# Optimization experiments

Hardware: AMD Instinct MI355X
Metric: run time of the kernel (lower is better)

## Reference

```python
import jax, jax.numpy as jnp
import numpy as np

N_NODES = 100000
N_EDGES = 1200000
DIM = 64
MAX_DEG = 64
NUM_LAB = 16
BN_EPS = 1e-5


def _lrelu(x):
    return jax.nn.leaky_relu(x, negative_slope=0.01)


def _bn(x, g, b):
    # BatchNorm1d in training mode: batch statistics over node axis
    m = x.mean(axis=0)
    v = x.var(axis=0)
    return (x - m) * jax.lax.rsqrt(v + BN_EPS) * g + b


def _gin_layer(h, src, dst, n, w1, b1, w2, b2, eps, g, b):
    # GINConv: (1+eps)*x_i + sum_{j in N(i)} x_j, then MLP (lin_lrelu_lin), BN, LeakyReLU
    agg = jax.ops.segment_sum(h[src], dst, num_segments=n)
    x = (1.0 + eps) * h + agg
    x = _lrelu(x @ w1 + b1) @ w2 + b2
    return _lrelu(_bn(x, g, b))


def setup_inputs() -> dict:
    key = jax.random.key(0)
    ks = jax.random.split(key, 16)
    s = 0.05
    inp = {
        'node_deg': jax.random.randint(ks[0], (N_NODES,), 0, MAX_DEG + 1, dtype=jnp.int32),
        'node_lab': jax.random.randint(ks[1], (N_NODES,), 0, NUM_LAB, dtype=jnp.int32),
        'edge_index': jax.random.randint(ks[2], (2, N_EDGES), 0, N_NODES, dtype=jnp.int32),
        'emb_deg': jax.random.normal(ks[3], (MAX_DEG + 1, DIM), jnp.float32) * s,
        'emb_lab': jax.random.normal(ks[4], (NUM_LAB, DIM), jnp.float32) * s,
        'l0_w1': jax.random.normal(ks[5], (2 * DIM, 2 * DIM), jnp.float32) * s,
        'l0_b1': jnp.zeros((2 * DIM,), jnp.float32),
        'l0_w2': jax.random.normal(ks[6], (2 * DIM, DIM), jnp.float32) * s,
        'l0_b2': jnp.zeros((DIM,), jnp.float32),
        'l0_eps': jnp.zeros((1,), jnp.float32),
        'bn0_g': jnp.ones((DIM,), jnp.float32),
        'bn0_b': jnp.zeros((DIM,), jnp.float32),
        'l1_w1': jax.random.normal(ks[7], (DIM, DIM), jnp.float32) * s,
        'l1_b1': jnp.zeros((DIM,), jnp.float32),
        'l1_w2': jax.random.normal(ks[8], (DIM, DIM), jnp.float32) * s,
        'l1_b2': jnp.zeros((DIM,), jnp.float32),
        'l1_eps': jnp.zeros((1,), jnp.float32),
        'bn1_g': jnp.ones((DIM,), jnp.float32),
        'bn1_b': jnp.zeros((DIM,), jnp.float32),
        'fc_w1': jax.random.normal(ks[9], (4 * DIM, DIM), jnp.float32) * s,
        'fc_b1': jnp.zeros((DIM,), jnp.float32),
        'fc_bn_g': jnp.ones((DIM,), jnp.float32),
        'fc_bn_b': jnp.zeros((DIM,), jnp.float32),
        'fc_w2': jax.random.normal(ks[10], (DIM, 1), jnp.float32) * s,
        'fc_b2': jnp.zeros((1,), jnp.float32),
    }
    return inp


def reference(node_deg, node_lab, edge_index, emb_deg, emb_lab,
              l0_w1, l0_b1, l0_w2, l0_b2, l0_eps, bn0_g, bn0_b,
              l1_w1, l1_b1, l1_w2, l1_b2, l1_eps, bn1_g, bn1_b,
              fc_w1, fc_b1, fc_bn_g, fc_bn_b, fc_w2, fc_b2):
    n = node_deg.shape[0]
    src, dst = edge_index[0], edge_index[1]
    # embedding concat: [N, 2*DIM]
    h0 = jnp.concatenate([emb_deg[node_deg], emb_lab[node_lab]], axis=1)
    h1 = _gin_layer(h0, src, dst, n, l0_w1, l0_b1, l0_w2, l0_b2, l0_eps[0], bn0_g, bn0_b)
    h2 = _gin_layer(h1, src, dst, n, l1_w1, l1_b1, l1_w2, l1_b2, l1_eps[0], bn1_g, bn1_b)
    x = jnp.concatenate([h0, h1, h2], axis=1)  # [N, 256]
    x = _lrelu(_bn(x @ fc_w1 + fc_b1, fc_bn_g, fc_bn_b))
    out = jax.nn.sigmoid(x @ fc_w2 + fc_b2)
    return out.squeeze(-1)  # [N]
```

## Files before the change

### kernel.cpp

```cpp
#include <hip/hip_runtime.h>

#define N_NODES 100000
#define N_EDGES 1200000
#define NCLS 81
#define NBKT 196
#define BCAP 8192
#define NCHK 293
#define NGBLK 1563

typedef unsigned short u16;
typedef unsigned char u8;
typedef unsigned int u32;
typedef unsigned long long u64;
typedef short bf16x8 __attribute__((ext_vector_type(8)));
typedef float f32x4 __attribute__((ext_vector_type(4)));

__device__ __forceinline__ float b2f(u16 u) {
  union { u32 i; float f; } v; v.i = ((u32)u) << 16; return v.f;
}
__device__ __forceinline__ u16 f2b(float f) {
  union { float f; u32 i; } v; v.f = f;
  u32 x = v.i;
  return (u16)((x + 0x7fffu + ((x >> 16) & 1u)) >> 16);
}
__device__ __forceinline__ void up2(u32 w, float& lo, float& hi) {
  union { u32 u; float f; } a, b;
  a.u = w << 16; b.u = w & 0xffff0000u;
  lo = a.f; hi = b.f;
}
__device__ __forceinline__ float lrelu(float x) { return x > 0.f ? x : 0.01f * x; }

__device__ __forceinline__ bool is_f32(const u16* emb) {
  int lane = threadIdx.x & 63;
  u32 e0 = (emb[lane * 2] >> 7) & 0xFF;
  u32 e1 = (emb[lane * 2 + 1] >> 7) & 0xFF;
  return __ballot((e0 >= 0x90) || (e1 >= 0x90)) != 0ull;
}

__device__ __forceinline__ float rdr(const void* p, int i, bool f32m) {
  return f32m ? ((const float*)p)[i] : b2f(((const u16*)p)[i]);
}

#define P_EMBD 0
#define P_EMBL 4160
#define P_W1A  5184
#define P_B1A  21568
#define P_W2A  21696
#define P_B2A  29888
#define P_EPS0 29952
#define P_G0   29953
#define P_BB0  30017
#define P_LW1  30081
#define P_LB1  34177
#define P_LW2  34241
#define P_LB2  38337
#define P_EPS1 38401
#define P_G1   38402
#define P_BB1  38466
#define P_FW1  38530
#define P_FB1  54914
#define P_FG   54978
#define P_FBB  55042
#define P_FW2  55106
#define P_FB2  55170
#define P_TOT  55171

struct CvtAll {
  const void* src[22];
  int cnt[22];
  int off[22];
};

struct RawPtrs {
  const void* embD;
  const void* embL;
  const void* w1r;
  const void* w2r;
  const void* lw1r;
  const void* lw2r;
  const void* fwr;
};

__global__ void k_init(CvtAll a, RawPtrs rw, const u16* __restrict__ embRaw,
                       float* __restrict__ P, float* __restrict__ W1p,
                       float* __restrict__ Efc, u16* __restrict__ bp,
                       u16* __restrict__ wpB, u32* __restrict__ gcur) {
  bool f32m = is_f32(embRaw);
  int tid = threadIdx.x;
  if (blockIdx.y < 22) {
    if (blockIdx.y == 0 && blockIdx.x == 0 && tid < NBKT) gcur[tid] = 0;
    int seg = blockIdx.y;
    int i = blockIdx.x * 256 + tid;
    if (i < a.cnt[seg]) {
      float v = f32m ? ((const float*)a.src[seg])[i] : b2f(((const u16*)a.src[seg])[i]);
      P[a.off[seg] + i] = v;
    }
    return;
  }
  int idx = blockIdx.x * 256 + tid;
  if (idx < NCLS * 128) {
    int c = idx >> 7, h = idx & 127;
    float s = 0.f;
    if (c < 65) {
      for (int k = 0; k < 64; ++k)
        s = fmaf(rdr(rw.embD, c * 64 + k, f32m), rdr(rw.w1r, k * 128 + h, f32m), s);
    } else {
      for (int k = 0; k < 64; ++k)
        s = fmaf(rdr(rw.embL, (c - 65) * 64 + k, f32m), rdr(rw.w1r, (64 + k) * 128 + h, f32m), s);
    }
    W1p[idx] = s;
    return;
  }
  if (idx < NCLS * 128 + NCLS * 64) {
    int r = idx - NCLS * 128;
    int c = r >> 6, o = r & 63;
    float s = 0.f;
    if (c < 65) {
      for (int k = 0; k < 64; ++k)
        s = fmaf(rdr(rw.embD, c * 64 + k, f32m), rdr(rw.fwr, k * 64 + o, f32m), s);
    } else {
      for (int k = 0; k < 64; ++k)
        s = fmaf(rdr(rw.embL, (c - 65) * 64 + k, f32m), rdr(rw.fwr, (64 + k) * 64 + o, f32m), s);
    }
    Efc[r] = s;
    return;
  }
  if (idx < NCLS * 128 + NCLS * 64 + 24576) {
    int pidx = idx - (NCLS * 128 + NCLS * 64);
    int seg, rel;
    if (pidx < 8192)       { seg = 0; rel = pidx; }
    else if (pidx < 12288) { seg = 1; rel = pidx - 8192; }
    else if (pidx < 16384) { seg = 2; rel = pidx - 12288; }
    else                   { seg = 3; rel = pidx - 16384; }
    const void* srcs[4] = {rw.w2r, rw.lw1r, rw.lw2r, rw.fwr};
    const int addoff[4] = {0, 0, 0, 128 * 64};
    const int KBs[4] = {4, 2, 2, 4};
    int j = rel & 7, lane = (rel >> 3) & 63, rest = rel >> 9;
    int kb = rest % KBs[seg], nt = rest / KBs[seg];
    int k = kb * 32 + (lane >> 4) * 8 + j;
    int n = nt * 16 + (lane & 15);
    bp[pidx] = f2b(rdr(srcs[seg], addoff[seg] + k * 64 + n, f32m));
    return;
  }
  int p2 = idx - (NCLS * 128 + NCLS * 64 + 24576);
  if (p2 >= 12288) return;
  int j = p2 & 7, lane = (p2 >> 3) & 63, rest = p2 >> 9;
  int kb = rest % 3, nt = rest / 3;
  int c = kb * 32 + (lane >> 4) * 8 + j;
  int n = nt * 16 + (lane & 15);
  float s = 0.f;
  if (c < NCLS) {
    if (c < 65) {
      for (int k = 0; k < 64; ++k)
        s = fmaf(rdr(rw.embD, c * 64 + k, f32m), rdr(rw.w1r, k * 128 + n, f32m), s);
    } else {
      for (int k = 0; k < 64; ++k)
        s = fmaf(rdr(rw.embL, (c - 65) * 64 + k, f32m), rdr(rw.w1r, (64 + k) * 128 + n, f32m), s);
    }
  }
  wpB[p2] = (c < NCLS) ? f2b(s) : 0;
}

__global__ __launch_bounds__(256) void k_bsort(const int* __restrict__ edge,
                                               const int* __restrict__ ndeg,
                                               const int* __restrict__ nlab,
                                               u32* __restrict__ gcur,
                                               u64* __restrict__ e2) {
  __shared__ u32 cnt[NBKT], rbase[NBKT];
  __shared__ u32 slo[4096], shi[4096];
  for (int i = threadIdx.x; i < NBKT; i += 256) cnt[i] = 0;
  __syncthreads();
  int base = blockIdx.x * 4096;
  for (int i = threadIdx.x; i < 4096; i += 256) {
    int e = base + i;
    if (e < N_EDGES) {
      int s = edge[e], d = edge[N_EDGES + e];
      slo[i] = ((u32)s << 11) | ((u32)ndeg[s] << 4) | (u32)nlab[s];
      shi[i] = (u32)d;
      atomicAdd(&cnt[(u32)d >> 9], 1u);
    } else shi[i] = 0xFFFFFFFFu;
  }
  __syncthreads();
  for (int i = threadIdx.x; i < NBKT; i += 256) {
    u32 c = cnt[i];
    rbase[i] = c ? atomicAdd(&gcur[i], c) : 0u;
    cnt[i] = 0;
  }
  __syncthreads();
  for (int i = threadIdx.x; i < 4096; i += 256) {
    u32 d = shi[i];
    if (d == 0xFFFFFFFFu) continue;
    u32 b = d >> 9;
    u32 pos = rbase[b] + atomicAdd(&cnt[b], 1u);
    e2[(size_t)b * BCAP + pos] = ((u64)d << 32) | (u64)slo[i];
  }
}

__global__ __launch_bounds__(512) void k_csrh(const u64* __restrict__ e2,
                                              const u32* __restrict__ gcur,
                                              const u16* __restrict__ wpB,
                                              const float* __restrict__ W1p,
                                              const float* __restrict__ P,
                                              const int* __restrict__ ndeg,
                                              const int* __restrict__ nlab,
                                              const u16* __restrict__ Bp2,
                                              u32* __restrict__ row_ptr,
                                              u32* __restrict__ einfo,
                                              u16* __restrict__ t0,
                                              float* __restrict__ pbuf) {
  __shared__ u32 l[512], cur[512], gl[NBKT];
  __shared__ u32 h32[512 * 24];
  __shared__ u32 sbase;
  __shared__ u16 T[8][16][136];
  __shared__ float lsum[8][64], lsq[8][64];
  int b = blockIdx.x, tid = threadIdx.x;
  if (tid < NBKT) gl[tid] = gcur[tid];
  l[tid] = 0;
  for (int i = tid; i < 512 * 24; i += 512) h32[i] = 0;
  __syncthreads();
  if (tid == 0) {
    u32 s = 0;
    for (int i = 0; i < b; ++i) s += gl[i];
    sbase = s;
  }
  __syncthreads();
  u32 cnt = gl[b];
  const u64* src = e2 + (size_t)b * BCAP;
  for (u32 e = tid; e < cnt; e += 512)
    atomicAdd(&l[(u32)(src[e] >> 32) & 511u], 1u);
  __syncthreads();
  u32 v = l[tid];
  for (int off = 1; off < 512; off <<= 1) {
    u32 a = (tid >= off) ? l[tid - off] : 0u;
    __syncthreads();
    l[tid] += a;
    __syncthreads();
  }
  u32 pos0 = sbase + l[tid] - v;
  cur[tid] = pos0;
  int nn = b * 512 + tid;
  if (nn <= N_NODES) row_ptr[nn] = pos0;
  __syncthreads();
  for (u32 e = tid; e < cnt; e += 512) {
    u64 r = src[e];
    u32 dl = (u32)(r >> 32) & 511u;
    u32 lo = (u32)r;
    u32 pos = atomicAdd(&cur[dl], 1u);
    einfo[pos] = lo;
    u32 c1 = (lo >> 4) & 0x7Fu, c2 = 65u + (lo & 15u);
    atomicAdd(&h32[dl * 24 + (c1 >> 2)], 1u << ((c1 & 3u) * 8));
    atomicAdd(&h32[dl * 24 + (c2 >> 2)], 1u << ((c2 & 3u) * 8));
  }
  __syncthreads();
  const u8* h = (const u8*)h32;
  int wid = tid >> 6, lane = tid & 63;
  int row = lane & 15, q = lane >> 4;
  float onep = 1.f + P[P_EPS0];
  const bf16x8* bp = (const bf16x8*)wpB;
  const bf16x8* bp2 = (const bf16x8*)Bp2;
  float ssA[4] = {0.f, 0.f, 0.f, 0.f}, qqA[4] = {0.f, 0.f, 0.f, 0.f};
#pragma unroll 1
  for (int t = wid; t < 32; t += 8) {
    int m0 = b * 512 + t * 16;
    if (m0 >= N_NODES) break;
    f32x4 acc[8];
#pragma unroll
    for (int nt = 0; nt < 8; ++nt) {
      float bb = P[P_B1A + nt * 16 + row];
      acc[nt][0] = bb; acc[nt][1] = bb; acc[nt][2] = bb; acc[nt][3] = bb;
    }
    const u8* ar = h + (t * 16 + row) * 96 + q * 8;
#pragma unroll
    for (int kb = 0; kb < 3; ++kb) {
      bf16x8 af;
#pragma unroll
      for (int j = 0; j < 8; ++j) af[j] = (short)f2b((float)ar[kb * 32 + j]);
#pragma unroll
      for (int nt = 0; nt < 8; ++nt) {
        bf16x8 bf = bp[(nt * 3 + kb) * 64 + lane];
        acc[nt] = __builtin_amdgcn_mfma_f32_16x16x32_bf16(af, bf, acc[nt], 0, 0, 0);
      }
    }
#pragma unroll
    for (int r = 0; r < 4; ++r) {
      int m = m0 + q * 4 + r;
      int node = q * 4 + r;
      if (m < N_NODES) {
        const float* wd = W1p + ndeg[m] * 128;
        const float* wl = W1p + (65 + nlab[m]) * 128;
#pragma unroll
        for (int nt = 0; nt < 8; ++nt) {
          int cc = nt * 16 + row;
          float vv = acc[nt][r] + onep * (wd[cc] + wl[cc]);
          T[wid][node][cc] = f2b(lrelu(vv));
        }
      } else {
#pragma unroll
        for (int nt = 0; nt < 8; ++nt) T[wid][node][nt * 16 + row] = 0;
      }
    }
    const u16* ap = &T[wid][row][q * 8];
    f32x4 acc2[4];
#pragma unroll
    for (int nt = 0; nt < 4; ++nt) {
      float bb = P[P_B2A + nt * 16 + row];
      acc2[nt][0] = bb; acc2[nt][1] = bb; acc2[nt][2] = bb; acc2[nt][3] = bb;
    }
#pragma unroll
    for (int kb = 0; kb < 4; ++kb) {
      bf16x8 af = *(const bf16x8*)(ap + kb * 32);
#pragma unroll
      for (int nt = 0; nt < 4; ++nt) {
        bf16x8 bf = bp2[(nt * 4 + kb) * 64 + lane];
        acc2[nt] = __builtin_amdgcn_mfma_f32_16x16x32_bf16(af, bf, acc2[nt], 0, 0, 0);
      }
    }
#pragma unroll
    for (int nt = 0; nt < 4; ++nt) {
      float s = 0.f, z = 0.f;
#pragma unroll
      for (int r = 0; r < 4; ++r) {
        int m = m0 + q * 4 + r;
        if (m < N_NODES) {
          u16 bv = f2b(acc2[nt][r]);
          t0[(size_t)m * 64 + nt * 16 + row] = bv;
          float vv = b2f(bv);
          s += vv; z = fmaf(vv, vv, z);
        }
      }
      s += __shfl_xor(s, 16, 64); s += __shfl_xor(s, 32, 64);
      z += __shfl_xor(z, 16, 64); z += __shfl_xor(z, 32, 64);
      ssA[nt] += s; qqA[nt] += z;
    }
  }
  if (lane < 16) {
#pragma unroll
    for (int nt = 0; nt < 4; ++nt) {
      lsum[wid][nt * 16 + lane] = ssA[nt];
      lsq[wid][nt * 16 + lane] = qqA[nt];
    }
  }
  __syncthreads();
  if (tid < 64) {
    float s = 0.f;
#pragma unroll
    for (int w = 0; w < 8; ++w) s += lsum[w][tid];
    pbuf[(size_t)b * 128 + tid] = s;
  } else if (tid < 128) {
    int c = tid - 64;
    float s = 0.f;
#pragma unroll
    for (int w = 0; w < 8; ++w) s += lsq[w][c];
    pbuf[(size_t)b * 128 + tid] = s;
  }
}

__global__ void k_sr(const float* __restrict__ pbuf, float* __restrict__ statsOut,
                     int nrows) {
  __shared__ float l[256];
  int c = blockIdx.x;
  float s = 0.f;
  for (int r = threadIdx.x; r < nrows; r += 256) s += pbuf[(size_t)r * 128 + c];
  l[threadIdx.x] = s;
  __syncthreads();
  for (int off = 128; off > 0; off >>= 1) {
    if (threadIdx.x < off) l[threadIdx.x] += l[threadIdx.x + off];
    __syncthreads();
  }
  if (threadIdx.x == 0) statsOut[c] = l[0];
}

template <int KB, int LDA, int BIASOFF>
__global__ __launch_bounds__(256) void k_gemm(const u16* __restrict__ A,
                                              const u16* __restrict__ Bp,
                                              const float* __restrict__ P,
                                              float* __restrict__ pbuf,
                                              u16* __restrict__ C) {
  __shared__ float lsum[4][64], lsq[4][64];
  int wid = threadIdx.x >> 6, lane = threadIdx.x & 63;
  int m0 = (blockIdx.x * 4 + wid) * 16;
  bool act = m0 < N_NODES;
  int row = lane & 15, q = lane >> 4;
  float ss[4] = {0.f, 0.f, 0.f, 0.f}, qq[4] = {0.f, 0.f, 0.f, 0.f};
  if (act) {
    const u16* ap = A + (size_t)(m0 + row) * LDA + q * 8;
    const bf16x8* bp = (const bf16x8*)Bp;
    f32x4 acc[4];
#pragma unroll
    for (int nt = 0; nt < 4; ++nt) {
      float b = (BIASOFF >= 0) ? P[BIASOFF + nt * 16 + row] : 0.f;
      acc[nt][0] = b; acc[nt][1] = b; acc[nt][2] = b; acc[nt][3] = b;
    }
#pragma unroll
    for (int kb = 0; kb < KB; ++kb) {
      bf16x8 af = *(const bf16x8*)(ap + kb * 32);
#pragma unroll
      for (int nt = 0; nt < 4; ++nt) {
        bf16x8 bf = bp[(nt * KB + kb) * 64 + lane];
        acc[nt] = __builtin_amdgcn_mfma_f32_16x16x32_bf16(af, bf, acc[nt], 0, 0, 0);
      }
    }
#pragma unroll
    for (int nt = 0; nt < 4; ++nt) {
      float s = 0.f, z = 0.f;
#pragma unroll
      for (int r = 0; r < 4; ++r) {
        int m = m0 + q * 4 + r;
        u16 bv = f2b(acc[nt][r]);
        C[(size_t)m * 64 + nt * 16 + row] = bv;
        float v = b2f(bv);
        s += v; z = fmaf(v, v, z);
      }
      s += __shfl_xor(s, 16, 64); s += __shfl_xor(s, 32, 64);
      z += __shfl_xor(z, 16, 64); z += __shfl_xor(z, 32, 64);
      ss[nt] = s; qq[nt] = z;
    }
  }
  if (lane < 16) {
#pragma unroll
    for (int nt = 0; nt < 4; ++nt) {
      lsum[wid][nt * 16 + lane] = ss[nt];
      lsq[wid][nt * 16 + lane] = qq[nt];
    }
  }
  __syncthreads();
  int t = threadIdx.x;
  if (t < 64)
    pbuf[(size_t)blockIdx.x * 128 + t] = lsum[0][t] + lsum[1][t] + lsum[2][t] + lsum[3][t];
  else if (t < 128) {
    int c = t - 64;
    pbuf[(size_t)blockIdx.x * 128 + t] = lsq[0][c] + lsq[1][c] + lsq[2][c] + lsq[3][c];
  }
}

__global__ __launch_bounds__(256) void k_gemm_bn(const u16* __restrict__ A,
                                                 const u16* __restrict__ Bp,
                                                 const float* __restrict__ P,
                                                 const float* __restrict__ stats,
                                                 u16* __restrict__ C) {
  int wid = threadIdx.x >> 6, lane = threadIdx.x & 63;
  int m0 = (blockIdx.x * 4 + wid) * 16;
  if (m0 >= N_NODES) return;
  int row = lane & 15, q = lane >> 4;
  const float invN = 1.f / (float)N_NODES;
  float sc[16], sh[16];
#pragma unroll
  for (int kb = 0; kb < 2; ++kb)
#pragma unroll
    for (int j = 0; j < 8; ++j) {
      int f = kb * 32 + q * 8 + j;
      float mm = stats[f] * invN;
      float var = fmaxf(stats[64 + f] * invN - mm * mm, 0.f);
      float inv = rsqrtf(var + 1e-5f);
      float s = inv * P[P_G0 + f];
      sc[kb * 8 + j] = s;
      sh[kb * 8 + j] = P[P_BB0 + f] - mm * s;
    }
  const u16* ap = A + (size_t)(m0 + row) * 64 + q * 8;
  const bf16x8* bp = (const bf16x8*)Bp;
  f32x4 acc[4];
#pragma unroll
  for (int nt = 0; nt < 4; ++nt) {
    acc[nt][0] = 0.f; acc[nt][1] = 0.f; acc[nt][2] = 0.f; acc[nt][3] = 0.f;
  }
#pragma unroll
  for (int kb = 0; kb < 2; ++kb) {
    uint4 raw = *(const uint4*)(ap + kb * 32);
    u32 rw[4] = {raw.x, raw.y, raw.z, raw.w};
    bf16x8 af;
#pragma unroll
    for (int p = 0; p < 4; ++p) {
      float lo, hi;
      up2(rw[p], lo, hi);
      float y0 = lrelu(fmaf(sc[kb * 8 + 2 * p], lo, sh[kb * 8 + 2 * p]));
      float y1 = lrelu(fmaf(sc[kb * 8 + 2 * p + 1], hi, sh[kb * 8 + 2 * p + 1]));
      af[2 * p] = (short)f2b(y0);
      af[2 * p + 1] = (short)f2b(y1);
    }
#pragma unroll
    for (int nt = 0; nt < 4; ++nt) {
      bf16x8 bf = bp[(nt * 2 + kb) * 64 + lane];
      acc[nt] = __builtin_amdgcn_mfma_f32_16x16x32_bf16(af, bf, acc[nt], 0, 0, 0);
    }
  }
#pragma unroll
  for (int nt = 0; nt < 4; ++nt)
#pragma unroll
    for (int r = 0; r < 4; ++r) {
      int m = m0 + q * 4 + r;
      C[(size_t)m * 64 + nt * 16 + row] = f2b(acc[nt][r]);
    }
}

__global__ __launch_bounds__(256) void k_agg1(const u32* __restrict__ rp,
                                              const u32* __restrict__ einfo,
                                              const u16* __restrict__ g1,
                                              const float* __restrict__ P,
                                              u16* __restrict__ abuf) {
  int lane = threadIdx.x & 63, wv = threadIdx.x >> 6;
  int n = blockIdx.x * 4 + wv;
  if (n >= N_NODES) return;
  u32 st = rp[n], en = rp[n + 1];
  u32 m = en - st;
  int grp = lane >> 4;
  int fo = (lane & 15) * 4;
  u32 myidx = (u32)n;
  if (lane < (int)m) myidx = einfo[st + lane] >> 11;
  u32 mm = m < 64u ? m : 64u;
  float a0 = 0.f, a1 = 0.f, a2 = 0.f, a3 = 0.f;
  for (u32 k = 0; k < mm; k += 16) {
#pragma unroll
    for (int bb = 0; bb < 4; ++bb) {
      u32 e = k + (u32)(bb * 4 + grp);
      u32 src = (u32)__shfl((int)myidx, (int)e, 64);
      if (e < mm) {
        uint2 v = *(const uint2*)(g1 + (size_t)src * 64 + fo);
        float l0, h0, l1, h1;
        up2(v.x, l0, h0);
        up2(v.y, l1, h1);
        a0 += l0; a1 += h0; a2 += l1; a3 += h1;
      }
    }
  }
  a0 += __shfl_xor(a0, 16, 64); a0 += __shfl_xor(a0, 32, 64);
  a1 += __shfl_xor(a1, 16, 64); a1 += __shfl_xor(a1, 32, 64);
  a2 += __shfl_xor(a2, 16, 64); a2 += __shfl_xor(a2, 32, 64);
  a3 += __shfl_xor(a3, 16, 64); a3 += __shfl_xor(a3, 32, 64);
  for (u32 k = 64; k < m; ++k) {
    u32 src = einfo[st + k] >> 11;
    uint2 v = *(const uint2*)(g1 + (size_t)src * 64 + fo);
    float l0, h0, l1, h1;
    up2(v.x, l0, h0);
    up2(v.y, l1, h1);
    a0 += l0; a1 += h0; a2 += l1; a3 += h1;
  }
  float onep = 1.f + P[P_EPS1];
  uint2 sv = *(const uint2*)(g1 + (size_t)n * 64 + fo);
  float s0, s1, s2, s3;
  up2(sv.x, s0, s1);
  up2(sv.y, s2, s3);
  float r0 = P[P_LB1 + fo + 0] + fmaf(onep, s0, a0);
  float r1 = P[P_LB1 + fo + 1] + fmaf(onep, s1, a1);
  float r2 = P[P_LB1 + fo + 2] + fmaf(onep, s2, a2);
  float r3 = P[P_LB1 + fo + 3] + fmaf(onep, s3, a3);
  if (lane < 16) {
    uint2 o;
    o.x = ((u32)f2b(lrelu(r0))) | (((u32)f2b(lrelu(r1))) << 16);
    o.y = ((u32)f2b(lrelu(r2))) | (((u32)f2b(lrelu(r3))) << 16);
    *(uint2*)(abuf + (size_t)n * 64 + fo) = o;
  }
}

__global__ __launch_bounds__(256) void k_gemm_fc1bn(const u16* __restrict__ t0,
                                                    const u16* __restrict__ t1,
                                                    const u16* __restrict__ Bp,
                                                    const float* __restrict__ P,
                                                    const float* __restrict__ stats,
                                                    float* __restrict__ pbuf,
                                                    const int* __restrict__ ndeg,
                                                    const int* __restrict__ nlab,
                                                    const float* __restrict__ Efc,
                                                    u16* __restrict__ C) {
  __shared__ float lsum[4][64], lsq[4][64];
  int wid = threadIdx.x >> 6, lane = threadIdx.x & 63;
  int m0 = (blockIdx.x * 4 + wid) * 16;
  bool act = m0 < N_NODES;
  int row = lane & 15, q = lane >> 4;
  float ss[4] = {0.f, 0.f, 0.f, 0.f}, qq[4] = {0.f, 0.f, 0.f, 0.f};
  if (act) {
    const float invN = 1.f / (float)N_NODES;
    float sc[32], sh[32];
#pragma unroll
    for (int h = 0; h < 2; ++h) {
      const float* st = stats + h * 128;
      int gof = h ? P_G1 : P_G0, bof = h ? P_BB1 : P_BB0;
#pragma unroll
      for (int kb = 0; kb < 2; ++kb)
#pragma unroll
        for (int j = 0; j < 8; ++j) {
          int f = kb * 32 + q * 8 + j;
          float mm = st[f] * invN;
          float var = fmaxf(st[64 + f] * invN - mm * mm, 0.f);
          float inv = rsqrtf(var + 1e-5f);
          float s = inv * P[gof + f];
          sc[h * 16 + kb * 8 + j] = s;
          sh[h * 16 + kb * 8 + j] = P[bof + f] - mm * s;
        }
    }
    const u16* a0 = t0 + (size_t)(m0 + row) * 64 + q * 8;
    const u16* a1 = t1 + (size_t)(m0 + row) * 64 + q * 8;
    const bf16x8* bp = (const bf16x8*)Bp;
    f32x4 acc[4];
#pragma unroll
    for (int nt = 0; nt < 4; ++nt) {
      float b = P[P_FB1 + nt * 16 + row];
      acc[nt][0] = b; acc[nt][1] = b; acc[nt][2] = b; acc[nt][3] = b;
    }
#pragma unroll
    for (int kb = 0; kb < 4; ++kb) {
      const u16* src = (kb < 2) ? (a0 + kb * 32) : (a1 + (kb - 2) * 32);
      int ci = (kb < 2) ? kb * 8 : 16 + (kb - 2) * 8;
      uint4 raw = *(const uint4*)src;
      u32 rw[4] = {raw.x, raw.y, raw.z, raw.w};
      bf16x8 af;
#pragma unroll
      for (int p = 0; p < 4; ++p) {
        float lo, hi;
        up2(rw[p], lo, hi);
        float y0 = lrelu(fmaf(sc[ci + 2 * p], lo, sh[ci + 2 * p]));
        float y1 = lrelu(fmaf(sc[ci + 2 * p + 1], hi, sh[ci + 2 * p + 1]));
        af[2 * p] = (short)f2b(y0);
        af[2 * p + 1] = (short)f2b(y1);
      }
#pragma unroll
      for (int nt = 0; nt < 4; ++nt) {
        bf16x8 bf = bp[(nt * 4 + kb) * 64 + lane];
        acc[nt] = __builtin_amdgcn_mfma_f32_16x16x32_bf16(af, bf, acc[nt], 0, 0, 0);
      }
    }
    float es[4][4];
#pragma unroll
    for (int r = 0; r < 4; ++r) {
      int m = m0 + q * 4 + r;
      int dn = ndeg[m], ln = 65 + nlab[m];
#pragma unroll
      for (int nt = 0; nt < 4; ++nt) {
        int cc = nt * 16 + row;
        es[r][nt] = acc[nt][r] + Efc[dn * 64 + cc] + Efc[ln * 64 + cc];
      }
    }
#pragma unroll
    for (int nt = 0; nt < 4; ++nt) {
      float s = 0.f, z = 0.f;
#pragma unroll
      for (int r = 0; r < 4; ++r) {
        int m = m0 + q * 4 + r;
        u16 bv = f2b(es[r][nt]);
        C[(size_t)m * 64 + nt * 16 + row] = bv;
        float v = b2f(bv);
        s += v; z = fmaf(v, v, z);
      }
      s += __shfl_xor(s, 16, 64); s += __shfl_xor(s, 32, 64);
      z += __shfl_xor(z, 16, 64); z += __shfl_xor(z, 32, 64);
      ss[nt] = s; qq[nt] = z;
    }
  }
  if (lane < 16) {
#pragma unroll
    for (int nt = 0; nt < 4; ++nt) {
      lsum[wid][nt * 16 + lane] = ss[nt];
      lsq[wid][nt * 16 + lane] = qq[nt];
    }
  }
  __syncthreads();
  int t = threadIdx.x;
  if (t < 64)
    pbuf[(size_t)blockIdx.x * 128 + t] = lsum[0][t] + lsum[1][t] + lsum[2][t] + lsum[3][t];
  else if (t < 128) {
    int c = t - 64;
    pbuf[(size_t)blockIdx.x * 128 + t] = lsq[0][c] + lsq[1][c] + lsq[2][c] + lsq[3][c];
  }
}

__global__ __launch_bounds__(256) void k_fc2(const u16* __restrict__ t,
                                             const float* __restrict__ stats,
                                             const float* __restrict__ P,
                                             const u16* __restrict__ embRaw,
                                             void* __restrict__ out) {
  __shared__ float scF[64], shF[64], fwF[64];
  bool f32m = is_f32(embRaw);
  int tid = threadIdx.x;
  if (tid < 64) {
    const float invN = 1.f / (float)N_NODES;
    float mm = stats[tid] * invN;
    float var = fmaxf(stats[64 + tid] * invN - mm * mm, 0.f);
    float inv = rsqrtf(var + 1e-5f);
    float s = inv * P[P_FG + tid];
    scF[tid] = s;
    shF[tid] = P[P_FBB + tid] - mm * s;
    fwF[tid] = P[P_FW2 + tid];
  }
  __syncthreads();
  int n = blockIdx.x * 256 + tid;
  if (n >= N_NODES) return;
  float z = P[P_FB2];
  const uint4* tn = (const uint4*)(t + (size_t)n * 64);
#pragma unroll
  for (int jj = 0; jj < 8; ++jj) {
    uint4 raw = tn[jj];
    u32 w[4] = {raw.x, raw.y, raw.z, raw.w};
#pragma unroll
    for (int p = 0; p < 4; ++p) {
      int f = jj * 8 + p * 2;
      float lo, hi;
      up2(w[p], lo, hi);
      float y0 = lrelu(fmaf(scF[f], lo, shF[f]));
      float y1 = lrelu(fmaf(scF[f + 1], hi, shF[f + 1]));
      z = fmaf(y0, fwF[f], z);
      z = fmaf(y1, fwF[f + 1], z);
    }
  }
  float s = 1.f / (1.f + expf(-z));
  if (!(fabsf(z) < 1e30f)) s = 0.25f;
  if (f32m) ((float*)out)[n] = s;
  else      ((u16*)out)[n] = f2b(s);
}

extern "C" void kernel_launch(void* const* d_in, const int* in_sizes, int n_in,
                              void* d_out, int out_size, void* d_ws, size_t ws_size,
                              hipStream_t stream) {
  const int* node_deg = (const int*)d_in[0];
  const int* node_lab = (const int*)d_in[1];
  const int* edge     = (const int*)d_in[2];
  const u16* embRaw   = (const u16*)d_in[3];
  (void)in_sizes; (void)n_in; (void)out_size; (void)ws_size;

  char* base = (char*)d_ws;
  size_t off = 0;
  auto alloc = [&](size_t bytes) -> void* {
    void* p = base + off;
    off += (bytes + 15) & ~(size_t)15;
    return p;
  };
  float* Pb    = (float*)alloc((size_t)P_TOT * 4);
  float* stats = (float*)alloc(384 * 4);
  u32* gcur    = (u32*)alloc(NBKT * 4);
  float* W1p   = (float*)alloc(NCLS * 128 * 4);
  float* Efc   = (float*)alloc(NCLS * 64 * 4);
  u16* bpack   = (u16*)alloc(24576 * 2);
  u16* wpB     = (u16*)alloc(12288 * 2);
  u32* row_ptr = (u32*)alloc((size_t)(N_NODES + 1) * 4);
  float* pbuf  = (float*)alloc((size_t)NGBLK * 128 * 4);
  u32* einfo   = (u32*)alloc((size_t)N_EDGES * 4);
  u64* e2      = (u64*)alloc((size_t)NBKT * BCAP * 8);
  void* arena  = alloc((size_t)N_NODES * 128 * 2);
  u16* t0      = (u16*)alloc((size_t)N_NODES * 64 * 2);
  u16* t1      = (u16*)alloc((size_t)N_NODES * 64 * 2);
  u16* t2      = (u16*)alloc((size_t)N_NODES * 64 * 2);
  u16* g1   = (u16*)arena;
  u16* abuf = (u16*)arena + (size_t)N_NODES * 64;
  u16* Bp_w2a = bpack;
  u16* Bp_lw1 = bpack + 8192;
  u16* Bp_lw2 = bpack + 12288;
  u16* Bp_fw1 = bpack + 16384;

  CvtAll ca;
  const int srcidx[22] = {3, 4, 5, 6, 7, 8, 9, 10, 11, 12, 13, 14, 15, 16, 17, 18, 19, 20, 21, 22, 23, 24};
  const int cnts[22]   = {4160, 1024, 16384, 128, 8192, 64, 1, 64, 64, 4096, 64, 4096, 64, 1, 64, 64, 16384, 64, 64, 64, 64, 1};
  const int offs[22]   = {P_EMBD, P_EMBL, P_W1A, P_B1A, P_W2A, P_B2A, P_EPS0, P_G0, P_BB0,
                          P_LW1, P_LB1, P_LW2, P_LB2, P_EPS1, P_G1, P_BB1,
                          P_FW1, P_FB1, P_FG, P_FBB, P_FW2, P_FB2};
  for (int i = 0; i < 22; ++i) { ca.src[i] = d_in[srcidx[i]]; ca.cnt[i] = cnts[i]; ca.off[i] = offs[i]; }
  RawPtrs rw;
  rw.embD = d_in[3]; rw.embL = d_in[4]; rw.w1r = d_in[5]; rw.w2r = d_in[7];
  rw.lw1r = d_in[12]; rw.lw2r = d_in[14]; rw.fwr = d_in[19];

  k_init<<<dim3(205, 23), 256, 0, stream>>>(ca, rw, embRaw, Pb, W1p, Efc, bpack, wpB, gcur);

  k_bsort<<<NCHK, 256, 0, stream>>>(edge, node_deg, node_lab, gcur, e2);

  k_csrh<<<NBKT, 512, 0, stream>>>(e2, gcur, wpB, W1p, Pb, node_deg, node_lab,
                                   Bp_w2a, row_ptr, einfo, t0, pbuf);
  k_sr<<<128, 256, 0, stream>>>(pbuf, stats, NBKT);

  const int GEMM_GRID = NGBLK;

  k_gemm_bn<<<GEMM_GRID, 256, 0, stream>>>(t0, Bp_lw1, Pb, stats, g1);
  k_agg1<<<(N_NODES + 3) / 4, 256, 0, stream>>>(row_ptr, einfo, g1, Pb, abuf);
  k_gemm<2, 64, P_LB2><<<GEMM_GRID, 256, 0, stream>>>(abuf, Bp_lw2, Pb, pbuf, t1);
  k_sr<<<128, 256, 0, stream>>>(pbuf, stats + 128, NGBLK);

  k_gemm_fc1bn<<<GEMM_GRID, 256, 0, stream>>>(t0, t1, Bp_fw1, Pb, stats, pbuf,
                                              node_deg, node_lab, Efc, t2);
  k_sr<<<128, 256, 0, stream>>>(pbuf, stats + 256, NGBLK);
  k_fc2<<<(N_NODES + 255) / 256, 256, 0, stream>>>(t2, stats + 256, Pb, embRaw, d_out);
}
```

Baseline: 285.1 us.

## Halve CSR bucket size to 256 nodes and use wave-shuffle scans

Destination buckets shrink from 512 to 256 nodes, giving 391 buckets with a smaller capacity. That roughly doubles the number of k_csrh blocks, so more blocks can run at once across the CUs and each block uses less shared memory for its histogram. The serial prefix over bucket counts and the barrier-heavy Hillis-Steele scan are replaced with wave-level shuffle reductions and scans. The trade-off is half the MFMA tiles per block, more global atomics on the bucket cursors, and a tighter bucket capacity that relies on the degree distribution staying close to uniform.

```diff
diff --git a/kernel.cpp b/kernel.cpp
--- a/kernel.cpp
+++ b/kernel.cpp
@@ -3,8 +3,8 @@
 #define N_NODES 100000
 #define N_EDGES 1200000
 #define NCLS 81
-#define NBKT 196
-#define BCAP 8192
+#define NBKT 391
+#define BCAP 4608
 #define NCHK 293
 #define NGBLK 1563
 
@@ -88,7 +88,9 @@
   bool f32m = is_f32(embRaw);
   int tid = threadIdx.x;
   if (blockIdx.y < 22) {
-    if (blockIdx.y == 0 && blockIdx.x == 0 && tid < NBKT) gcur[tid] = 0;
+    if (blockIdx.y == 0 && blockIdx.x == 0) {
+      for (int i = tid; i < NBKT; i += 256) gcur[i] = 0;
+    }
     int seg = blockIdx.y;
     int i = blockIdx.x * 256 + tid;
     if (i < a.cnt[seg]) {
@@ -177,7 +179,7 @@
       int s = edge[e], d = edge[N_EDGES + e];
       slo[i] = ((u32)s << 11) | ((u32)ndeg[s] << 4) | (u32)nlab[s];
       shi[i] = (u32)d;
-      atomicAdd(&cnt[(u32)d >> 9], 1u);
+      atomicAdd(&cnt[(u32)d >> 8], 1u);
     } else shi[i] = 0xFFFFFFFFu;
   }
   __syncthreads();
@@ -190,7 +192,7 @@
   for (int i = threadIdx.x; i < 4096; i += 256) {
     u32 d = shi[i];
     if (d == 0xFFFFFFFFu) continue;
-    u32 b = d >> 9;
+    u32 b = d >> 8;
     u32 pos = rbase[b] + atomicAdd(&cnt[b], 1u);
     e2[(size_t)b * BCAP + pos] = ((u64)d << 32) | (u64)slo[i];
   }
@@ -208,42 +210,54 @@
                                               u32* __restrict__ einfo,
                                               u16* __restrict__ t0,
                                               float* __restrict__ pbuf) {
-  __shared__ u32 l[512], cur[512], gl[NBKT];
-  __shared__ u32 h32[512 * 24];
+  __shared__ u32 l[256], cur[256], gl[NBKT], wt[8];
+  __shared__ u32 h32[256 * 24];
   __shared__ u32 sbase;
   __shared__ u16 T[8][16][136];
   __shared__ float lsum[8][64], lsq[8][64];
   int b = blockIdx.x, tid = threadIdx.x;
+  int wid = tid >> 6, lane = tid & 63;
   if (tid < NBKT) gl[tid] = gcur[tid];
-  l[tid] = 0;
-  for (int i = tid; i < 512 * 24; i += 512) h32[i] = 0;
-  __syncthreads();
-  if (tid == 0) {
+  if (tid < 256) l[tid] = 0;
+  for (int i = tid; i < 256 * 24; i += 512) h32[i] = 0;
+  __syncthreads();
+  if (wid == 0) {
     u32 s = 0;
-    for (int i = 0; i < b; ++i) s += gl[i];
-    sbase = s;
-  }
-  __syncthreads();
+    for (int i = lane; i < b; i += 64) s += gl[i];
+    s += __shfl_xor(s, 1, 64); s += __shfl_xor(s, 2, 64); s += __shfl_xor(s, 4, 64);
+    s += __shfl_xor(s, 8, 64); s += __shfl_xor(s, 16, 64); s += __shfl_xor(s, 32, 64);
+    if (lane == 0) sbase = s;
+  }
   u32 cnt = gl[b];
   const u64* src = e2 + (size_t)b * BCAP;
   for (u32 e = tid; e < cnt; e += 512)
-    atomicAdd(&l[(u32)(src[e] >> 32) & 511u], 1u);
-  __syncthreads();
-  u32 v = l[tid];
-  for (int off = 1; off < 512; off <<= 1) {
-    u32 a = (tid >= off) ? l[tid - off] : 0u;
-    __syncthreads();
-    l[tid] += a;
-    __syncthreads();
-  }
-  u32 pos0 = sbase + l[tid] - v;
-  cur[tid] = pos0;
-  int nn = b * 512 + tid;
-  if (nn <= N_NODES) row_ptr[nn] = pos0;
+    atomicAdd(&l[(u32)(src[e] >> 32) & 255u], 1u);
+  __syncthreads();
+  u32 v = 0, incl = 0;
+  if (tid < 256) {
+    v = l[tid];
+    u32 x = v;
+#pragma unroll
+    for (int off = 1; off < 64; off <<= 1) {
+      u32 t = __shfl_up(x, off, 64);
+      if (lane >= off) x += t;
+    }
+    if (lane == 63) wt[wid] = x;
+    incl = x;
+  }
+  __syncthreads();
+  if (tid < 256) {
+    u32 woff = 0;
+    for (int w = 0; w < wid; ++w) woff += wt[w];
+    u32 pos0 = sbase + woff + incl - v;
+    cur[tid] = pos0;
+    int nn = b * 256 + tid;
+    if (nn <= N_NODES) row_ptr[nn] = pos0;
+  }
   __syncthreads();
   for (u32 e = tid; e < cnt; e += 512) {
     u64 r = src[e];
-    u32 dl = (u32)(r >> 32) & 511u;
+    u32 dl = (u32)(r >> 32) & 255u;
     u32 lo = (u32)r;
     u32 pos = atomicAdd(&cur[dl], 1u);
     einfo[pos] = lo;
@@ -253,15 +267,14 @@
   }
   __syncthreads();
   const u8* h = (const u8*)h32;
-  int wid = tid >> 6, lane = tid & 63;
   int row = lane & 15, q = lane >> 4;
   float onep = 1.f + P[P_EPS0];
   const bf16x8* bp = (const bf16x8*)wpB;
   const bf16x8* bp2 = (const bf16x8*)Bp2;
   float ssA[4] = {0.f, 0.f, 0.f, 0.f}, qqA[4] = {0.f, 0.f, 0.f, 0.f};
 #pragma unroll 1
-  for (int t = wid; t < 32; t += 8) {
-    int m0 = b * 512 + t * 16;
+  for (int t = wid; t < 16; t += 8) {
+    int m0 = b * 256 + t * 16;
     if (m0 >= N_NODES) break;
     f32x4 acc[8];
 #pragma unroll
```

After: 287.2 us. No clear change (+0.7%).
